# Optimization experiments

Hardware: AMD Instinct MI355X
Metric: run time of the kernel (lower is better)

The kernel has to match this reference:

```python
import jax, jax.numpy as jnp
import numpy as np

N_NODES = 20000
N_EDGES = 320000
INDIM = 64
OUTDIM = 128
EDGE_DIM = 16
HEADS = 4
ED = OUTDIM // 2          # encoded edge dim = 64
C1 = 2 * INDIM // HEADS   # 32 -> concat 128
C2 = OUTDIM // HEADS      # 32 -> concat 128
C3 = 2 * OUTDIM // HEADS  # 64 -> concat 256


def setup_inputs() -> dict:
    key = jax.random.key(0)
    ks = iter(jax.random.split(key, 80))
    def p(*shape):
        return jax.random.normal(next(ks), shape, dtype=jnp.float32) * 0.05
    inp = {}
    inp['x_in'] = jax.random.normal(next(ks), (N_NODES, INDIM), dtype=jnp.float32)
    inp['edge_index'] = jax.random.randint(next(ks), (2, N_EDGES), 0, N_NODES)
    inp['edge_attr'] = jax.random.normal(next(ks), (N_EDGES, EDGE_DIM), dtype=jnp.float32)
    # BatchNorm1d (eval mode: running stats)
    inp['bn0_g'] = jnp.ones(INDIM, jnp.float32) + p(INDIM)
    inp['bn0_b'] = p(INDIM)
    inp['bn0_m'] = p(INDIM)
    inp['bn0_v'] = jnp.ones(INDIM, jnp.float32) + 0.1 * jax.random.uniform(next(ks), (INDIM,))
    # edge encoder: Linear(edge_dim,outdim) -> LeakyReLU -> Linear(outdim,outdim//2) -> LeakyReLU
    inp['ee_W1'] = p(EDGE_DIM, OUTDIM); inp['ee_b1'] = p(OUTDIM)
    inp['ee_W2'] = p(OUTDIM, ED); inp['ee_b2'] = p(ED)
    # GATv2 layers: lin_l, lin_r (bias), lin_edge (no bias), att [H,C], out bias [H*C]
    def gat_params(prefix, din, C):
        inp[prefix + '_Wl'] = p(din, HEADS * C); inp[prefix + '_bl'] = p(HEADS * C)
        inp[prefix + '_Wr'] = p(din, HEADS * C); inp[prefix + '_br'] = p(HEADS * C)
        inp[prefix + '_We'] = p(ED, HEADS * C)
        inp[prefix + '_att'] = p(HEADS, C)
        inp[prefix + '_bias'] = p(HEADS * C)
    gat_params('g1', INDIM, C1)
    gat_params('g2', HEADS * C1, C2)
    gat_params('g3', HEADS * C2, C3)
    # LayerNorms
    inp['ln1_g'] = jnp.ones(HEADS * C1, jnp.float32); inp['ln1_b'] = p(HEADS * C1)
    inp['ln2_g'] = jnp.ones(HEADS * C2, jnp.float32); inp['ln2_b'] = p(HEADS * C2)
    inp['ln3_g'] = jnp.ones(HEADS * C3, jnp.float32); inp['ln3_b'] = p(HEADS * C3)
    # skip / mixing / heads
    inp['skip_W'] = p(INDIM, HEADS * C1); inp['skip_b'] = p(HEADS * C1)
    inp['alpha_p'] = jnp.float32(0.3)
    inp['fp_W'] = p(HEADS * C1, HEADS * C3); inp['fp_b'] = p(HEADS * C3)
    catout = HEADS * C3
    inp['np_W1'] = p(catout, catout // 2); inp['np_b1'] = p(catout // 2)
    inp['np_W2'] = p(catout // 2, catout // 4); inp['np_b2'] = p(catout // 4)
    inp['np_W3'] = p(catout // 4, 1); inp['np_b3'] = p(1)
    return inp


def _ln(x, g, b):
    m = jnp.mean(x, axis=-1, keepdims=True)
    v = jnp.var(x, axis=-1, keepdims=True)
    return (x - m) / jnp.sqrt(v + 1e-5) * g + b


def _gatv2(x, src, dst, ea, Wl, bl, Wr, br, We, att, bias, N):
    # GATv2Conv (eval): e = att . leaky_relu(x_j + x_i + e_ij, 0.2); segment softmax over dst
    H, C = att.shape
    xl = (x @ Wl + bl).reshape(N, H, C)   # source transform
    xr = (x @ Wr + br).reshape(N, H, C)   # target transform
    ee = (ea @ We).reshape(-1, H, C)      # edge transform (no bias)
    m = jax.nn.leaky_relu(xl[src] + xr[dst] + ee, 0.2)  # [E,H,C]
    e = jnp.einsum('ehc,hc->eh', m, att)
    emax = jax.ops.segment_max(e, dst, num_segments=N)
    ex = jnp.exp(e - emax[dst])
    den = jax.ops.segment_sum(ex, dst, num_segments=N)
    alpha = ex / (den[dst] + 1e-16)       # [E,H]
    out = jax.ops.segment_sum(xl[src] * alpha[:, :, None], dst, num_segments=N)
    return out.reshape(N, H * C) + bias, alpha


def reference(x_in, edge_index, edge_attr, bn0_g, bn0_b, bn0_m, bn0_v,
              ee_W1, ee_b1, ee_W2, ee_b2,
              g1_Wl, g1_bl, g1_Wr, g1_br, g1_We, g1_att, g1_bias,
              g2_Wl, g2_bl, g2_Wr, g2_br, g2_We, g2_att, g2_bias,
              g3_Wl, g3_bl, g3_Wr, g3_br, g3_We, g3_att, g3_bias,
              ln1_g, ln1_b, ln2_g, ln2_b, ln3_g, ln3_b,
              skip_W, skip_b, alpha_p, fp_W, fp_b,
              np_W1, np_b1, np_W2, np_b2, np_W3, np_b3):
    N = x_in.shape[0]
    # BatchNorm1d eval
    x = (x_in - bn0_m) / jnp.sqrt(bn0_v + 1e-5) * bn0_g + bn0_b
    # edge encoder + L2 normalize
    ea = jax.nn.leaky_relu(edge_attr @ ee_W1 + ee_b1, 0.01)
    ea = jax.nn.leaky_relu(ea @ ee_W2 + ee_b2, 0.01)
    ea = ea / jnp.maximum(jnp.linalg.norm(ea, axis=-1, keepdims=True), 1e-12)
    # add self loops (fill_value='mean' of incoming encoded edge_attr)
    src0, dst0 = edge_index[0], edge_index[1]
    deg = jax.ops.segment_sum(jnp.ones_like(ea[:, 0]), dst0, num_segments=N)
    loop_attr = jax.ops.segment_sum(ea, dst0, num_segments=N) / jnp.maximum(deg, 1.0)[:, None]
    ar = jnp.arange(N, dtype=src0.dtype)
    src = jnp.concatenate([src0, ar]); dst = jnp.concatenate([dst0, ar])
    ea2 = jnp.concatenate([ea, loop_attr], axis=0)
    x1, a1 = _gatv2(x, src, dst, ea2, g1_Wl, g1_bl, g1_Wr, g1_br, g1_We, g1_att, g1_bias, N)
    x1 = jax.nn.leaky_relu(_ln(x1, ln1_g, ln1_b), 0.01)
    skip1 = 0.01 * (x @ skip_W + skip_b) + x1  # skip_weight = 0.01 (frozen)
    x2, a2 = _gatv2(skip1, src, dst, ea2, g2_Wl, g2_bl, g2_Wr, g2_br, g2_We, g2_att, g2_bias, N)
    x2 = jax.nn.leaky_relu(_ln(x2, ln2_g, ln2_b), 0.01)
    x3, a3 = _gatv2(x2, src, dst, ea2, g3_Wl, g3_bl, g3_Wr, g3_br, g3_We, g3_att, g3_bias, N)
    x3 = jax.nn.leaky_relu(_ln(x3, ln3_g, ln3_b), 0.01)
    s = jax.nn.sigmoid(alpha_p)
    xf = s * (x1 @ fp_W + fp_b) + (1.0 - s) * x3
    h = jax.nn.elu(xf @ np_W1 + np_b1)
    h = jax.nn.elu(h @ np_W2 + np_b2)
    node_probs = h @ np_W3 + np_b3
    return (xf, node_probs, a1, a2, a3)
```

## Files before the change

kernel.cpp:

```cpp
#include <hip/hip_runtime.h>
#include <math.h>

#define DEV __device__ __forceinline__

typedef __attribute__((ext_vector_type(8))) short bf16x8;
typedef __attribute__((ext_vector_type(4))) float f32x4;

DEV float leakyf(float x, float s) { return x > 0.f ? x : s * x; }

DEV unsigned short f2bf(float f) {
  unsigned u = __float_as_uint(f);
  unsigned r = (u + 0x7fff + ((u >> 16) & 1)) >> 16;
  return (unsigned short)r;
}
DEV float bf2f(unsigned short h) { return __uint_as_float((unsigned)h << 16); }

DEV float sel4(float4 v, int h) {
  float a = (h & 1) ? v.y : v.x;
  float b = (h & 1) ? v.w : v.z;
  return (h & 2) ? b : a;
}

DEV float wave_sum(float v) {
#pragma unroll
  for (int o = 1; o < 64; o <<= 1) v += __shfl_xor(v, o);
  return v;
}
DEV float wave_max(float v) {
#pragma unroll
  for (int o = 1; o < 64; o <<= 1) v = fmaxf(v, __shfl_xor(v, o));
  return v;
}

struct WJob { const float* in; unsigned short* out; int K; int Nc; };
struct WJobs { WJob j[13]; };

__global__ __launch_bounds__(256) void wt_kernel(WJobs jobs) {
  WJob jb = jobs.j[blockIdx.y];
  int total = jb.K * jb.Nc;
  for (int i = blockIdx.x * 256 + threadIdx.x; i < total; i += gridDim.x * 256) {
    int c = i / jb.K, k = i - c * jb.K;
    jb.out[i] = f2bf(jb.in[(size_t)k * jb.Nc + c]);
  }
}

__global__ __launch_bounds__(256) void bn_kernel(
    const float* __restrict__ xin, const float* __restrict__ g,
    const float* __restrict__ b, const float* __restrict__ m,
    const float* __restrict__ v, float* __restrict__ xout, int total) {
  int i = blockIdx.x * 256 + threadIdx.x;
  if (i < total) {
    int c = i & 63;
    xout[i] = (xin[i] - m[c]) * rsqrtf(v[c] + 1e-5f) * g[c] + b[c];
  }
}

__global__ __launch_bounds__(256) void edge_enc_kernel(
    const float* __restrict__ edge_attr, const unsigned short* __restrict__ WT1,
    const float* __restrict__ b1, const unsigned short* __restrict__ WT2,
    const float* __restrict__ b2, unsigned short* __restrict__ ea_bf, int E) {
  __shared__ __align__(16) unsigned short sEa1[64][136];
  int tid = threadIdx.x, lane = tid & 63, w = tid >> 6;
  int g = lane >> 4, q = lane & 15;
  bf16x8 w1f[8];
#pragma unroll
  for (int t = 0; t < 8; t++) {
    bf16x8 v = {};
    if (g < 2) v = *(const bf16x8*)(WT1 + (size_t)(16 * t + q) * 16 + 8 * g);
    w1f[t] = v;
  }
  float b1v[8];
#pragma unroll
  for (int t = 0; t < 8; t++) b1v[t] = b1[16 * t + q];
  bf16x8 w2f[4][4];
#pragma unroll
  for (int t = 0; t < 4; t++)
#pragma unroll
    for (int kc = 0; kc < 4; kc++)
      w2f[t][kc] = *(const bf16x8*)(WT2 + (size_t)(16 * t + q) * 128 + 32 * kc + 8 * g);
  float b2v[4];
#pragma unroll
  for (int t = 0; t < 4; t++) b2v[t] = b2[16 * t + q];

  int gstride = gridDim.x * 64;

  auto load_attr = [&](int base) -> bf16x8 {
    bf16x8 af = {};
    if (g < 2) {
      int e = base + w * 16 + q;
      if (e >= E) e = E - 1;
      const float* ap = edge_attr + (size_t)e * 16 + 8 * g;
      float4 x0 = *(const float4*)ap;
      float4 x1 = *(const float4*)(ap + 4);
      af[0] = (short)f2bf(x0.x); af[1] = (short)f2bf(x0.y);
      af[2] = (short)f2bf(x0.z); af[3] = (short)f2bf(x0.w);
      af[4] = (short)f2bf(x1.x); af[5] = (short)f2bf(x1.y);
      af[6] = (short)f2bf(x1.z); af[7] = (short)f2bf(x1.w);
    }
    return af;
  };

  int base = blockIdx.x * 64;
  if (base >= E) return;
  bf16x8 af = load_attr(base);
  for (; base < E; ) {
    int next = base + gstride;
    bf16x8 af_next = {};
    if (next < E) af_next = load_attr(next);
    f32x4 acc1[8];
#pragma unroll
    for (int t = 0; t < 8; t++) acc1[t] = (f32x4){0.f, 0.f, 0.f, 0.f};
#pragma unroll
    for (int t = 0; t < 8; t++)
      acc1[t] = __builtin_amdgcn_mfma_f32_16x16x32_bf16(af, w1f[t], acc1[t], 0, 0, 0);
#pragma unroll
    for (int t = 0; t < 8; t++)
#pragma unroll
      for (int r = 0; r < 4; r++) {
        float v = leakyf(acc1[t][r] + b1v[t], 0.01f);
        sEa1[w * 16 + g * 4 + r][16 * t + q] = f2bf(v);
      }
    f32x4 acc2[4];
#pragma unroll
    for (int t = 0; t < 4; t++) acc2[t] = (f32x4){0.f, 0.f, 0.f, 0.f};
#pragma unroll
    for (int kc = 0; kc < 4; kc++) {
      bf16x8 a2 = *(const bf16x8*)&sEa1[w * 16 + q][32 * kc + 8 * g];
#pragma unroll
      for (int t = 0; t < 4; t++)
        acc2[t] = __builtin_amdgcn_mfma_f32_16x16x32_bf16(a2, w2f[t][kc], acc2[t], 0, 0, 0);
    }
#pragma unroll
    for (int r = 0; r < 4; r++) {
      float vv[4];
      float p = 0.f;
#pragma unroll
      for (int t = 0; t < 4; t++) {
        float v = leakyf(acc2[t][r] + b2v[t], 0.01f);
        vv[t] = v;
        p += v * v;
      }
#pragma unroll
      for (int o = 1; o < 16; o <<= 1) p += __shfl_xor(p, o);
      float sc = 1.f / fmaxf(sqrtf(p), 1e-12f);
#pragma unroll
      for (int t = 0; t < 4; t++)
        sEa1[w * 16 + g * 4 + r][16 * t + q] = f2bf(vv[t] * sc);
    }
#pragma unroll
    for (int p = 0; p < 2; p++) {
      int rl = p * 8 + (lane >> 3);
      int e = base + w * 16 + rl;
      if (e < E) {
        bf16x8 v = *(const bf16x8*)&sEa1[w * 16 + rl][(lane & 7) * 8];
        *(bf16x8*)(ea_bf + (size_t)e * 64 + (lane & 7) * 8) = v;
      }
    }
    af = af_next;
    base = next;
  }
}

__global__ __launch_bounds__(256) void count_kernel(const int* __restrict__ dst0,
                                                    int* __restrict__ counts, int E, int E2) {
  int i = blockIdx.x * 256 + threadIdx.x;
  if (i < E2) {
    int d = (i < E) ? dst0[i] : (i - E);
    atomicAdd(&counts[d], 1);
  }
}

__global__ __launch_bounds__(1024) void scan_kernel(const int* __restrict__ counts,
                                                    int* __restrict__ rowptr,
                                                    int* __restrict__ fill, int N) {
  __shared__ int part[1024];
  int tid = threadIdx.x;
  int chunk = (N + 1023) / 1024;
  int lo = tid * chunk, hi = lo + chunk;
  if (hi > N) hi = N;
  if (lo > N) lo = N;
  int s = 0;
  for (int i = lo; i < hi; i++) s += counts[i];
  part[tid] = s;
  __syncthreads();
#pragma unroll
  for (int o = 1; o < 1024; o <<= 1) {
    int v = (tid >= o) ? part[tid - o] : 0;
    __syncthreads();
    part[tid] += v;
    __syncthreads();
  }
  if (tid == 1023) rowptr[N] = part[1023];
  int off = part[tid] - s;
  for (int i = lo; i < hi; i++) {
    rowptr[i] = off;
    fill[i] = off;
    off += counts[i];
  }
}

__global__ __launch_bounds__(256) void fill_kernel(const int* __restrict__ src0,
                                                   const int* __restrict__ dst0,
                                                   int* __restrict__ fill,
                                                   int* __restrict__ csr,
                                                   int* __restrict__ srcpos,
                                                   int* __restrict__ dstpos, int E, int E2) {
  int i = blockIdx.x * 256 + threadIdx.x;
  if (i < E2) {
    int d, s;
    if (i < E) {
      d = dst0[i];
      s = src0[i];
    } else {
      d = s = i - E;
    }
    int pos = atomicAdd(&fill[d], 1);
    csr[pos] = i;
    srcpos[pos] = s;
    dstpos[pos] = d;
  }
}

__global__ __launch_bounds__(256) void loopattr_kernel(unsigned short* __restrict__ ea_bf,
                                                       const int* __restrict__ rowptr,
                                                       const int* __restrict__ csr, int N, int E) {
  int lane = threadIdx.x & 63, wv = threadIdx.x >> 6;
  int stride = gridDim.x * 4;
  for (int n = blockIdx.x * 4 + wv; n < N; n += stride) {
    int r0 = rowptr[n], r1 = rowptr[n + 1];
    float acc = 0.f;
    int cnt = 0;
    for (int i = r0; i < r1; i++) {
      int e = csr[i];
      if (e < E) {
        acc += bf2f(ea_bf[(size_t)e * 64 + lane]);
        cnt++;
      }
    }
    ea_bf[((size_t)E + n) * 64 + lane] = f2bf(acc / fmaxf((float)cnt, 1.f));
  }
}

template <int MODE>
__global__ __launch_bounds__(256) void gemm_mfma_kernel(
    const float* __restrict__ A, const unsigned short* __restrict__ BT,
    const float* __restrict__ bias, void* __restrict__ Cout, int M, int K, int Nc,
    const float* __restrict__ aux, const float* __restrict__ alpha_p) {
  __shared__ unsigned short sA[64][40];
  __shared__ unsigned short sB[64][40];
  int tid = threadIdx.x, lane = tid & 63, w = tid >> 6;
  int g = lane >> 4, q = lane & 15;
  int bm = blockIdx.y * 64, bn = blockIdx.x * 64;
  f32x4 acc[4];
#pragma unroll
  for (int t = 0; t < 4; t++) acc[t] = (f32x4){0.f, 0.f, 0.f, 0.f};
  int r = tid >> 2, ko = (tid & 3) * 8;
  for (int k0 = 0; k0 < K; k0 += 32) {
    {
      int gm = bm + r;
      bf16x8 v = {};
      if (gm < M) {
        const float* ap = A + (size_t)gm * K + k0 + ko;
        float4 x0 = *(const float4*)ap;
        float4 x1 = *(const float4*)(ap + 4);
        v[0] = (short)f2bf(x0.x); v[1] = (short)f2bf(x0.y);
        v[2] = (short)f2bf(x0.z); v[3] = (short)f2bf(x0.w);
        v[4] = (short)f2bf(x1.x); v[5] = (short)f2bf(x1.y);
        v[6] = (short)f2bf(x1.z); v[7] = (short)f2bf(x1.w);
      }
      *(bf16x8*)&sA[r][ko] = v;
      int gc = bn + r;
      bf16x8 bv = {};
      if (gc < Nc) bv = *(const bf16x8*)(BT + (size_t)gc * K + k0 + ko);
      *(bf16x8*)&sB[r][ko] = bv;
    }
    __syncthreads();
    bf16x8 a = *(const bf16x8*)&sA[w * 16 + q][8 * g];
#pragma unroll
    for (int t = 0; t < 4; t++) {
      bf16x8 b = *(const bf16x8*)&sB[16 * t + q][8 * g];
      acc[t] = __builtin_amdgcn_mfma_f32_16x16x32_bf16(a, b, acc[t], 0, 0, 0);
    }
    __syncthreads();
  }
  float s = 0.f;
  if (MODE == 3) s = 1.f / (1.f + __expf(-alpha_p[0]));
#pragma unroll
  for (int t = 0; t < 4; t++) {
    int col = bn + 16 * t + q;
#pragma unroll
    for (int rr = 0; rr < 4; rr++) {
      int row = bm + w * 16 + g * 4 + rr;
      if (row < M && col < Nc) {
        float v = acc[t][rr] + bias[col];
        if (MODE == 2) v = v > 0.f ? v : (__expf(v) - 1.f);
        if (MODE == 3) v = s * v + (1.f - s) * aux[(size_t)row * Nc + col];
        if (MODE == 1)
          ((unsigned short*)Cout)[(size_t)row * Nc + col] = f2bf(v);
        else
          ((float*)Cout)[(size_t)row * Nc + col] = v;
      }
    }
  }
}

struct GJob { const unsigned short* BT; const float* bias; void* out; int mode; };
struct GJobs { GJob j[3]; };

__global__ __launch_bounds__(256) void gemm_mfma_batched(
    const float* __restrict__ A, GJobs jobs, int M, int K, int Nc) {
  __shared__ unsigned short sA[64][40];
  __shared__ unsigned short sB[64][40];
  GJob jb = jobs.j[blockIdx.z];
  const unsigned short* BT = jb.BT;
  int tid = threadIdx.x, lane = tid & 63, w = tid >> 6;
  int g = lane >> 4, q = lane & 15;
  int bm = blockIdx.y * 64, bn = blockIdx.x * 64;
  f32x4 acc[4];
#pragma unroll
  for (int t = 0; t < 4; t++) acc[t] = (f32x4){0.f, 0.f, 0.f, 0.f};
  int r = tid >> 2, ko = (tid & 3) * 8;
  for (int k0 = 0; k0 < K; k0 += 32) {
    {
      int gm = bm + r;
      bf16x8 v = {};
      if (gm < M) {
        const float* ap = A + (size_t)gm * K + k0 + ko;
        float4 x0 = *(const float4*)ap;
        float4 x1 = *(const float4*)(ap + 4);
        v[0] = (short)f2bf(x0.x); v[1] = (short)f2bf(x0.y);
        v[2] = (short)f2bf(x0.z); v[3] = (short)f2bf(x0.w);
        v[4] = (short)f2bf(x1.x); v[5] = (short)f2bf(x1.y);
        v[6] = (short)f2bf(x1.z); v[7] = (short)f2bf(x1.w);
      }
      *(bf16x8*)&sA[r][ko] = v;
      int gc = bn + r;
      bf16x8 bv = {};
      if (gc < Nc) bv = *(const bf16x8*)(BT + (size_t)gc * K + k0 + ko);
      *(bf16x8*)&sB[r][ko] = bv;
    }
    __syncthreads();
    bf16x8 a = *(const bf16x8*)&sA[w * 16 + q][8 * g];
#pragma unroll
    for (int t = 0; t < 4; t++) {
      bf16x8 b = *(const bf16x8*)&sB[16 * t + q][8 * g];
      acc[t] = __builtin_amdgcn_mfma_f32_16x16x32_bf16(a, b, acc[t], 0, 0, 0);
    }
    __syncthreads();
  }
#pragma unroll
  for (int t = 0; t < 4; t++) {
    int col = bn + 16 * t + q;
#pragma unroll
    for (int rr = 0; rr < 4; rr++) {
      int row = bm + w * 16 + g * 4 + rr;
      if (row < M && col < Nc) {
        float v = acc[t][rr] + jb.bias[col];
        if (jb.mode == 1)
          ((unsigned short*)jb.out)[(size_t)row * Nc + col] = f2bf(v);
        else
          ((float*)jb.out)[(size_t)row * Nc + col] = v;
      }
    }
  }
}

template <int C>
__global__ __launch_bounds__(256) void score_mfma_kernel(
    const unsigned short* __restrict__ ea_bf, const unsigned short* __restrict__ xl,
    const unsigned short* __restrict__ xr, const float* __restrict__ We,
    const float* __restrict__ att, const int* __restrict__ csr,
    const int* __restrict__ srcpos, const int* __restrict__ dstpos,
    float* __restrict__ e_s, int E2, int HCfull, int col_off) {
  int lane = threadIdx.x & 63;
  int wv = threadIdx.x >> 6;
  int g = lane >> 4, q = lane & 15;
  bf16x8 bfrag[8][2];
#pragma unroll
  for (int t = 0; t < 8; t++)
#pragma unroll
    for (int kc = 0; kc < 2; kc++) {
      bf16x8 bv;
#pragma unroll
      for (int j = 0; j < 8; j++) {
        int k = kc * 32 + g * 8 + j;
        bv[j] = (short)f2bf(We[(size_t)k * HCfull + col_off + 16 * t + q]);
      }
      bfrag[t][kc] = bv;
    }
  float attv[8];
#pragma unroll
  for (int t = 0; t < 8; t++) attv[t] = att[col_off + 16 * t + q];

  constexpr int TPH = C / 16;
  constexpr int NH = 8 / TPH;
  const int headbase = col_off / C;

  int tiles = (E2 + 15) / 16;
  int nw = gridDim.x * 4;
  for (int tile = blockIdx.x * 4 + wv; tile < tiles; tile += nw) {
    int i0 = tile * 16;
    int ia = i0 + q;
    if (ia >= E2) ia = E2 - 1;
    int erow = csr[ia];
    const unsigned short* ap = ea_bf + (size_t)erow * 64 + g * 8;
    bf16x8 a0 = *(const bf16x8*)(ap);
    bf16x8 a1 = *(const bf16x8*)(ap + 32);
    f32x4 acc[8];
#pragma unroll
    for (int t = 0; t < 8; t++) acc[t] = (f32x4){0.f, 0.f, 0.f, 0.f};
#pragma unroll
    for (int t = 0; t < 8; t++) {
      acc[t] = __builtin_amdgcn_mfma_f32_16x16x32_bf16(a0, bfrag[t][0], acc[t], 0, 0, 0);
      acc[t] = __builtin_amdgcn_mfma_f32_16x16x32_bf16(a1, bfrag[t][1], acc[t], 0, 0, 0);
    }
    int sn[4], dn[4];
#pragma unroll
    for (int r = 0; r < 4; r++) {
      int i = i0 + g * 4 + r;
      if (i >= E2) i = E2 - 1;
      sn[r] = srcpos[i];
      dn[r] = dstpos[i];
    }
    float p[NH][4];
#pragma unroll
    for (int hh = 0; hh < NH; hh++)
#pragma unroll
      for (int r = 0; r < 4; r++) p[hh][r] = 0.f;
#pragma unroll
    for (int t = 0; t < 8; t++) {
      int col = col_off + 16 * t + q;
#pragma unroll
      for (int r = 0; r < 4; r++) {
        float xv = bf2f(xl[(size_t)sn[r] * HCfull + col]) +
                   bf2f(xr[(size_t)dn[r] * HCfull + col]) + acc[t][r];
        xv = xv > 0.f ? xv : 0.2f * xv;
        p[t / TPH][r] += xv * attv[t];
      }
    }
#pragma unroll
    for (int hh = 0; hh < NH; hh++)
#pragma unroll
      for (int r = 0; r < 4; r++) {
#pragma unroll
        for (int o = 1; o < 16; o <<= 1) p[hh][r] += __shfl_xor(p[hh][r], o);
      }
    if (q == 0) {
#pragma unroll
      for (int r = 0; r < 4; r++) {
        int i = i0 + g * 4 + r;
        if (i < E2) {
#pragma unroll
          for (int hh = 0; hh < NH; hh++)
            e_s[(size_t)i * 4 + headbase + hh] = p[hh][r];
        }
      }
    }
  }
}

template <int HC, bool L1MODE>
__global__ __launch_bounds__(256) void aggr_kernel(
    const float* __restrict__ e_s, const unsigned short* __restrict__ xl,
    const int* __restrict__ rowptr, const int* __restrict__ srcpos,
    const float* __restrict__ bias,
    const float* __restrict__ lng, const float* __restrict__ lnb,
    float* __restrict__ xout,
    float* __restrict__ x1out, const float* __restrict__ skipproj,
    float* __restrict__ md, int N) {
  constexpr int CPL = HC / 64;
  int lane = threadIdx.x & 63, wv = threadIdx.x >> 6;
  int stride = gridDim.x * 4;
  const float4* e_s4 = (const float4*)e_s;
  for (int n = blockIdx.x * 4 + wv; n < N; n += stride) {
    int r0 = rowptr[n], r1 = rowptr[n + 1];
    float m0 = -1e30f, m1 = -1e30f, m2 = -1e30f, m3 = -1e30f;
    for (int i = r0 + lane; i < r1; i += 64) {
      float4 v = e_s4[i];
      m0 = fmaxf(m0, v.x);
      m1 = fmaxf(m1, v.y);
      m2 = fmaxf(m2, v.z);
      m3 = fmaxf(m3, v.w);
    }
    m0 = wave_max(m0);
    m1 = wave_max(m1);
    m2 = wave_max(m2);
    m3 = wave_max(m3);
    float d0 = 0.f, d1 = 0.f, d2 = 0.f, d3 = 0.f;
    for (int i = r0 + lane; i < r1; i += 64) {
      float4 v = e_s4[i];
      d0 += __expf(v.x - m0);
      d1 += __expf(v.y - m1);
      d2 += __expf(v.z - m2);
      d3 += __expf(v.w - m3);
    }
    d0 = wave_sum(d0);
    d1 = wave_sum(d1);
    d2 = wave_sum(d2);
    d3 = wave_sum(d3);
    float i0 = 1.f / (d0 + 1e-16f), i1 = 1.f / (d1 + 1e-16f);
    float i2 = 1.f / (d2 + 1e-16f), i3 = 1.f / (d3 + 1e-16f);
    if (lane == 0) {
      float* mp = md + (size_t)n * 8;
      mp[0] = m0; mp[1] = m1; mp[2] = m2; mp[3] = m3;
      mp[4] = i0; mp[5] = i1; mp[6] = i2; mp[7] = i3;
    }
    int h = lane >> 4;
    float mh = (h & 2) ? ((h & 1) ? m3 : m2) : ((h & 1) ? m1 : m0);
    float ih = (h & 2) ? ((h & 1) ? i3 : i2) : ((h & 1) ? i1 : i0);
    float acc[CPL];
#pragma unroll
    for (int j = 0; j < CPL; j++) acc[j] = 0.f;
    int c0 = lane * CPL;
    int i = r0;
    for (; i + 4 <= r1; i += 4) {
      float sh0, sh1, sh2, sh3;
      int sn0, sn1, sn2, sn3;
      {
        float4 a = e_s4[i], b = e_s4[i + 1], c = e_s4[i + 2], d = e_s4[i + 3];
        sh0 = sel4(a, h); sh1 = sel4(b, h); sh2 = sel4(c, h); sh3 = sel4(d, h);
      }
      sn0 = srcpos[i]; sn1 = srcpos[i + 1]; sn2 = srcpos[i + 2]; sn3 = srcpos[i + 3];
      if constexpr (CPL == 2) {
        ushort2 t0 = *(const ushort2*)(xl + (size_t)sn0 * HC + c0);
        ushort2 t1 = *(const ushort2*)(xl + (size_t)sn1 * HC + c0);
        ushort2 t2 = *(const ushort2*)(xl + (size_t)sn2 * HC + c0);
        ushort2 t3 = *(const ushort2*)(xl + (size_t)sn3 * HC + c0);
        float a0 = __expf(sh0 - mh) * ih;
        float a1 = __expf(sh1 - mh) * ih;
        float a2 = __expf(sh2 - mh) * ih;
        float a3 = __expf(sh3 - mh) * ih;
        acc[0] += a0 * bf2f(t0.x) + a1 * bf2f(t1.x) + a2 * bf2f(t2.x) + a3 * bf2f(t3.x);
        acc[1] += a0 * bf2f(t0.y) + a1 * bf2f(t1.y) + a2 * bf2f(t2.y) + a3 * bf2f(t3.y);
      } else {
        ushort4 t0 = *(const ushort4*)(xl + (size_t)sn0 * HC + c0);
        ushort4 t1 = *(const ushort4*)(xl + (size_t)sn1 * HC + c0);
        ushort4 t2 = *(const ushort4*)(xl + (size_t)sn2 * HC + c0);
        ushort4 t3 = *(const ushort4*)(xl + (size_t)sn3 * HC + c0);
        float a0 = __expf(sh0 - mh) * ih;
        float a1 = __expf(sh1 - mh) * ih;
        float a2 = __expf(sh2 - mh) * ih;
        float a3 = __expf(sh3 - mh) * ih;
        acc[0] += a0 * bf2f(t0.x) + a1 * bf2f(t1.x) + a2 * bf2f(t2.x) + a3 * bf2f(t3.x);
        acc[1] += a0 * bf2f(t0.y) + a1 * bf2f(t1.y) + a2 * bf2f(t2.y) + a3 * bf2f(t3.y);
        acc[2] += a0 * bf2f(t0.z) + a1 * bf2f(t1.z) + a2 * bf2f(t2.z) + a3 * bf2f(t3.z);
        acc[3] += a0 * bf2f(t0.w) + a1 * bf2f(t1.w) + a2 * bf2f(t2.w) + a3 * bf2f(t3.w);
      }
    }
    for (; i < r1; i++) {
      float sh = sel4(e_s4[i], h);
      float a = __expf(sh - mh) * ih;
      int sn = srcpos[i];
      const unsigned short* xp = xl + (size_t)sn * HC + c0;
      if constexpr (CPL == 2) {
        ushort2 t = *(const ushort2*)xp;
        acc[0] += a * bf2f(t.x);
        acc[1] += a * bf2f(t.y);
      } else {
        ushort4 t = *(const ushort4*)xp;
        acc[0] += a * bf2f(t.x);
        acc[1] += a * bf2f(t.y);
        acc[2] += a * bf2f(t.z);
        acc[3] += a * bf2f(t.w);
      }
    }
    float vals[CPL];
    float vs = 0.f, vq = 0.f;
#pragma unroll
    for (int j = 0; j < CPL; j++) {
      float t = acc[j] + bias[c0 + j];
      vals[j] = t;
      vs += t;
      vq += t * t;
    }
    vs = wave_sum(vs);
    vq = wave_sum(vq);
    float mean = vs * (1.f / HC);
    float var = vq * (1.f / HC) - mean * mean;
    float rstd = rsqrtf(fmaxf(var, 0.f) + 1e-5f);
#pragma unroll
    for (int j = 0; j < CPL; j++) {
      int c = c0 + j;
      float y = (vals[j] - mean) * rstd * lng[c] + lnb[c];
      y = leakyf(y, 0.01f);
      if constexpr (L1MODE) {
        x1out[(size_t)n * HC + c] = y;
        xout[(size_t)n * HC + c] = 0.01f * skipproj[(size_t)n * HC + c] + y;
      } else {
        xout[(size_t)n * HC + c] = y;
      }
    }
  }
}

__global__ __launch_bounds__(256) void alpha_kernel(
    const float* __restrict__ e_s, const int* __restrict__ csr,
    const int* __restrict__ dstpos, const float* __restrict__ md,
    float* __restrict__ alpha_out, int E2) {
  int i = blockIdx.x * 256 + threadIdx.x;
  if (i < E2) {
    float4 sv = ((const float4*)e_s)[i];
    int d = dstpos[i];
    const float* mp = md + (size_t)d * 8;
    float4 a;
    a.x = __expf(sv.x - mp[0]) * mp[4];
    a.y = __expf(sv.y - mp[1]) * mp[5];
    a.z = __expf(sv.z - mp[2]) * mp[6];
    a.w = __expf(sv.w - mp[3]) * mp[7];
    ((float4*)alpha_out)[csr[i]] = a;
  }
}

extern "C" void kernel_launch(void* const* d_in, const int* in_sizes, int n_in,
                              void* d_out, int out_size, void* d_ws, size_t ws_size,
                              hipStream_t stream) {
  (void)n_in;
  (void)out_size;
  (void)ws_size;
  const float* x_in = (const float*)d_in[0];
  const int* edge_index = (const int*)d_in[1];
  const float* edge_attr = (const float*)d_in[2];
  const float* bn0_g = (const float*)d_in[3];
  const float* bn0_b = (const float*)d_in[4];
  const float* bn0_m = (const float*)d_in[5];
  const float* bn0_v = (const float*)d_in[6];
  const float* eeW1 = (const float*)d_in[7];
  const float* eeb1 = (const float*)d_in[8];
  const float* eeW2 = (const float*)d_in[9];
  const float* eeb2 = (const float*)d_in[10];
  const float* g1_Wl = (const float*)d_in[11];
  const float* g1_bl = (const float*)d_in[12];
  const float* g1_Wr = (const float*)d_in[13];
  const float* g1_br = (const float*)d_in[14];
  const float* g1_We = (const float*)d_in[15];
  const float* g1_att = (const float*)d_in[16];
  const float* g1_bias = (const float*)d_in[17];
  const float* g2_Wl = (const float*)d_in[18];
  const float* g2_bl = (const float*)d_in[19];
  const float* g2_Wr = (const float*)d_in[20];
  const float* g2_br = (const float*)d_in[21];
  const float* g2_We = (const float*)d_in[22];
  const float* g2_att = (const float*)d_in[23];
  const float* g2_bias = (const float*)d_in[24];
  const float* g3_Wl = (const float*)d_in[25];
  const float* g3_bl = (const float*)d_in[26];
  const float* g3_Wr = (const float*)d_in[27];
  const float* g3_br = (const float*)d_in[28];
  const float* g3_We = (const float*)d_in[29];
  const float* g3_att = (const float*)d_in[30];
  const float* g3_bias = (const float*)d_in[31];
  const float* ln1_g = (const float*)d_in[32];
  const float* ln1_b = (const float*)d_in[33];
  const float* ln2_g = (const float*)d_in[34];
  const float* ln2_b = (const float*)d_in[35];
  const float* ln3_g = (const float*)d_in[36];
  const float* ln3_b = (const float*)d_in[37];
  const float* skip_W = (const float*)d_in[38];
  const float* skip_b = (const float*)d_in[39];
  const float* alpha_p = (const float*)d_in[40];
  const float* fp_W = (const float*)d_in[41];
  const float* fp_b = (const float*)d_in[42];
  const float* np_W1 = (const float*)d_in[43];
  const float* np_b1 = (const float*)d_in[44];
  const float* np_W2 = (const float*)d_in[45];
  const float* np_b2 = (const float*)d_in[46];
  const float* np_W3 = (const float*)d_in[47];
  const float* np_b3 = (const float*)d_in[48];

  const int N = in_sizes[0] / 64;
  const int E = in_sizes[2] / 16;
  const int E2 = E + N;
  const int* src0 = edge_index;
  const int* dst0 = edge_index + E;

  float* ws = (float*)d_ws;
  size_t off = 0;
  float* x = ws + off;         off += (size_t)N * 64;
  unsigned short* ea_bf = (unsigned short*)(ws + off); off += (size_t)E2 * 32;
  unsigned short* xl = (unsigned short*)(ws + off);    off += (size_t)N * 128;
  unsigned short* xr = (unsigned short*)(ws + off);    off += (size_t)N * 128;
  float* skipproj = ws + off;  off += (size_t)N * 128;
  float* x1 = ws + off;        off += (size_t)N * 128;
  float* skip1 = ws + off;     off += (size_t)N * 128;
  float* x2 = ws + off;        off += (size_t)N * 128;
  float* x3 = ws + off;        off += (size_t)N * 256;
  float* e_s = ws + off;       off += (size_t)E2 * 4;
  float* h2 = ws + off;        off += (size_t)N * 64;
  float* md = ws + off;        off += (size_t)N * 8;
  int* counts = (int*)(ws + off);
  int* rowptr = counts + N;
  int* fill = rowptr + N + 1;
  int* csr = fill + N;
  int* srcpos = csr + E2;
  int* dstpos = srcpos + E2;
  off += (size_t)(3 * N + 1 + 3 * E2);
  off = (off + 3) & ~(size_t)3;
  unsigned short* wtp = (unsigned short*)(ws + off);
  auto alloc_wt = [&](int elems) {
    unsigned short* p = wtp;
    wtp += (elems + 7) & ~7;
    return p;
  };
  unsigned short* wt_g1l = alloc_wt(64 * 128);
  unsigned short* wt_g1r = alloc_wt(64 * 128);
  unsigned short* wt_skip = alloc_wt(64 * 128);
  unsigned short* wt_g2l = alloc_wt(128 * 128);
  unsigned short* wt_g2r = alloc_wt(128 * 128);
  unsigned short* wt_g3l = alloc_wt(128 * 256);
  unsigned short* wt_g3r = alloc_wt(128 * 256);
  unsigned short* wt_fp = alloc_wt(128 * 256);
  unsigned short* wt_np1 = alloc_wt(256 * 128);
  unsigned short* wt_np2 = alloc_wt(128 * 64);
  unsigned short* wt_np3 = alloc_wt(64 * 1);
  unsigned short* wt_ee1 = alloc_wt(16 * 128);
  unsigned short* wt_ee2 = alloc_wt(128 * 64);

  float* out = (float*)d_out;
  float* xf = out;
  float* npout = out + (size_t)N * 256;
  float* a1 = npout + N;
  float* a2 = a1 + (size_t)E2 * 4;
  float* a3 = a2 + (size_t)E2 * 4;

  WJobs jobs;
  jobs.j[0] = {g1_Wl, wt_g1l, 64, 128};
  jobs.j[1] = {g1_Wr, wt_g1r, 64, 128};
  jobs.j[2] = {skip_W, wt_skip, 64, 128};
  jobs.j[3] = {g2_Wl, wt_g2l, 128, 128};
  jobs.j[4] = {g2_Wr, wt_g2r, 128, 128};
  jobs.j[5] = {g3_Wl, wt_g3l, 128, 256};
  jobs.j[6] = {g3_Wr, wt_g3r, 128, 256};
  jobs.j[7] = {fp_W, wt_fp, 128, 256};
  jobs.j[8] = {np_W1, wt_np1, 256, 128};
  jobs.j[9] = {np_W2, wt_np2, 128, 64};
  jobs.j[10] = {np_W3, wt_np3, 64, 1};
  jobs.j[11] = {eeW1, wt_ee1, 16, 128};
  jobs.j[12] = {eeW2, wt_ee2, 128, 64};

  hipMemsetAsync(counts, 0, (size_t)N * sizeof(int), stream);
  wt_kernel<<<dim3(64, 13), 256, 0, stream>>>(jobs);
  bn_kernel<<<(N * 64 + 255) / 256, 256, 0, stream>>>(x_in, bn0_g, bn0_b, bn0_m, bn0_v, x, N * 64);
  edge_enc_kernel<<<2560, 256, 0, stream>>>(edge_attr, wt_ee1, eeb1, wt_ee2, eeb2, ea_bf, E);
  count_kernel<<<(E2 + 255) / 256, 256, 0, stream>>>(dst0, counts, E, E2);
  scan_kernel<<<1, 1024, 0, stream>>>(counts, rowptr, fill, N);
  fill_kernel<<<(E2 + 255) / 256, 256, 0, stream>>>(src0, dst0, fill, csr, srcpos, dstpos, E, E2);
  loopattr_kernel<<<(N + 3) / 4, 256, 0, stream>>>(ea_bf, rowptr, csr, N, E);

  auto gemm = [&](int mode, const float* A, const unsigned short* BT, const float* bias,
                  void* Cp, int M, int K, int Nc, const float* aux) {
    dim3 gdim((Nc + 63) / 64, (M + 63) / 64);
    switch (mode) {
      case 0: gemm_mfma_kernel<0><<<gdim, 256, 0, stream>>>(A, BT, bias, Cp, M, K, Nc, nullptr, nullptr); break;
      case 2: gemm_mfma_kernel<2><<<gdim, 256, 0, stream>>>(A, BT, bias, Cp, M, K, Nc, nullptr, nullptr); break;
      case 3: gemm_mfma_kernel<3><<<gdim, 256, 0, stream>>>(A, BT, bias, Cp, M, K, Nc, aux, alpha_p); break;
    }
  };
  auto gemm_batch = [&](const float* A, int M, int K, int Nc, GJobs gj, int nz) {
    dim3 gdim((Nc + 63) / 64, (M + 63) / 64, nz);
    gemm_mfma_batched<<<gdim, 256, 0, stream>>>(A, gj, M, K, Nc);
  };

  const int nblk_node = (N + 3) / 4;
  const int score_blocks = 1024;
  const int nblk_edge = (E2 + 255) / 256;

  {
    GJobs gj;
    gj.j[0] = {wt_g1l, g1_bl, xl, 1};
    gj.j[1] = {wt_g1r, g1_br, xr, 1};
    gj.j[2] = {wt_skip, skip_b, skipproj, 0};
    gemm_batch(x, N, 64, 128, gj, 3);
  }
  score_mfma_kernel<32><<<score_blocks, 256, 0, stream>>>(ea_bf, xl, xr, g1_We, g1_att, csr, srcpos, dstpos, e_s, E2, 128, 0);
  aggr_kernel<128, true><<<nblk_node, 256, 0, stream>>>(e_s, xl, rowptr, srcpos, g1_bias, ln1_g, ln1_b,
                                                        skip1, x1, skipproj, md, N);
  alpha_kernel<<<nblk_edge, 256, 0, stream>>>(e_s, csr, dstpos, md, a1, E2);
  {
    GJobs gj;
    gj.j[0] = {wt_g2l, g2_bl, xl, 1};
    gj.j[1] = {wt_g2r, g2_br, xr, 1};
    gj.j[2] = {nullptr, nullptr, nullptr, 0};
    gemm_batch(skip1, N, 128, 128, gj, 2);
  }
  score_mfma_kernel<32><<<score_blocks, 256, 0, stream>>>(ea_bf, xl, xr, g2_We, g2_att, csr, srcpos, dstpos, e_s, E2, 128, 0);
  aggr_kernel<128, false><<<nblk_node, 256, 0, stream>>>(e_s, xl, rowptr, srcpos, g2_bias, ln2_g, ln2_b,
                                                         x2, nullptr, nullptr, md, N);
  alpha_kernel<<<nblk_edge, 256, 0, stream>>>(e_s, csr, dstpos, md, a2, E2);
  {
    GJobs gj;
    gj.j[0] = {wt_g3l, g3_bl, xl, 1};
    gj.j[1] = {wt_g3r, g3_br, xr, 1};
    gj.j[2] = {nullptr, nullptr, nullptr, 0};
    gemm_batch(x2, N, 128, 256, gj, 2);
  }
  score_mfma_kernel<64><<<score_blocks, 256, 0, stream>>>(ea_bf, xl, xr, g3_We, g3_att, csr, srcpos, dstpos, e_s, E2, 256, 0);
  score_mfma_kernel<64><<<score_blocks, 256, 0, stream>>>(ea_bf, xl, xr, g3_We, g3_att, csr, srcpos, dstpos, e_s, E2, 256, 128);
  aggr_kernel<256, false><<<nblk_node, 256, 0, stream>>>(e_s, xl, rowptr, srcpos, g3_bias, ln3_g, ln3_b,
                                                         x3, nullptr, nullptr, md, N);
  alpha_kernel<<<nblk_edge, 256, 0, stream>>>(e_s, csr, dstpos, md, a3, E2);
  gemm(3, x1, wt_fp, fp_b, xf, N, 128, 256, x3);
  gemm(2, xf, wt_np1, np_b1, skipproj, N, 256, 128, nullptr);
  gemm(2, skipproj, wt_np2, np_b2, h2, N, 128, 64, nullptr);
  gemm(0, h2, wt_np3, np_b3, npout, N, 64, 1, nullptr);
}
```

Baseline: 530.5 us.

## Merge layer-3 score kernels into one split launch and simplify edge encoder output

Layer 3's two score launches, one per 128-column half, become a single launch. In it, wave pairs cover the two column halves of the same edge tile, so both halves share the gathered edge attributes and node features in cache. The edge encoder now writes normalized outputs straight to global memory with scalar bf16 stores instead of staging them through shared memory for vectorized stores. It also gets a launch-bounds occupancy hint and half the grid size. The direct stores are narrow and less coalesced, which could cost more than the dropped shared-memory round trip saves.

```diff
diff --git a/kernel.cpp b/kernel.cpp
--- a/kernel.cpp
+++ b/kernel.cpp
@@ -55,11 +55,11 @@
   }
 }
 
-__global__ __launch_bounds__(256) void edge_enc_kernel(
+__global__ __launch_bounds__(256, 2) void edge_enc_kernel(
     const float* __restrict__ edge_attr, const unsigned short* __restrict__ WT1,
     const float* __restrict__ b1, const unsigned short* __restrict__ WT2,
     const float* __restrict__ b2, unsigned short* __restrict__ ea_bf, int E) {
-  __shared__ __align__(16) unsigned short sEa1[64][136];
+  __shared__ unsigned short sEa1[64][136];
   int tid = threadIdx.x, lane = tid & 63, w = tid >> 6;
   int g = lane >> 4, q = lane & 15;
   bf16x8 w1f[8];
@@ -107,6 +107,7 @@
     int next = base + gstride;
     bf16x8 af_next = {};
     if (next < E) af_next = load_attr(next);
+    int e0 = base + w * 16;
     f32x4 acc1[8];
 #pragma unroll
     for (int t = 0; t < 8; t++) acc1[t] = (f32x4){0.f, 0.f, 0.f, 0.f};
@@ -143,17 +144,11 @@
 #pragma unroll
       for (int o = 1; o < 16; o <<= 1) p += __shfl_xor(p, o);
       float sc = 1.f / fmaxf(sqrtf(p), 1e-12f);
-#pragma unroll
-      for (int t = 0; t < 4; t++)
-        sEa1[w * 16 + g * 4 + r][16 * t + q] = f2bf(vv[t] * sc);
-    }
-#pragma unroll
-    for (int p = 0; p < 2; p++) {
-      int rl = p * 8 + (lane >> 3);
-      int e = base + w * 16 + rl;
+      int e = e0 + g * 4 + r;
       if (e < E) {
-        bf16x8 v = *(const bf16x8*)&sEa1[w * 16 + rl][(lane & 7) * 8];
-        *(bf16x8*)(ea_bf + (size_t)e * 64 + (lane & 7) * 8) = v;
+#pragma unroll
+        for (int t = 0; t < 4; t++)
+          ea_bf[(size_t)e * 64 + 16 * t + q] = f2bf(vv[t] * sc);
       }
     }
     af = af_next;
@@ -365,16 +360,17 @@
   }
 }
 
-template <int C>
+template <int C, bool SPLIT>
 __global__ __launch_bounds__(256) void score_mfma_kernel(
     const unsigned short* __restrict__ ea_bf, const unsigned short* __restrict__ xl,
     const unsigned short* __restrict__ xr, const float* __restrict__ We,
     const float* __restrict__ att, const int* __restrict__ csr,
     const int* __restrict__ srcpos, const int* __restrict__ dstpos,
-    float* __restrict__ e_s, int E2, int HCfull, int col_off) {
+    float* __restrict__ e_s, int E2, int HCfull, int col_off_in) {
   int lane = threadIdx.x & 63;
   int wv = threadIdx.x >> 6;
   int g = lane >> 4, q = lane & 15;
+  int col_off = SPLIT ? (wv & 1) * 128 : col_off_in;
   bf16x8 bfrag[8][2];
 #pragma unroll
   for (int t = 0; t < 8; t++)
@@ -397,8 +393,9 @@
   const int headbase = col_off / C;
 
   int tiles = (E2 + 15) / 16;
-  int nw = gridDim.x * 4;
-  for (int tile = blockIdx.x * 4 + wv; tile < tiles; tile += nw) {
+  int tstart = SPLIT ? (blockIdx.x * 2 + (wv >> 1)) : (blockIdx.x * 4 + wv);
+  int nw = SPLIT ? (gridDim.x * 2) : (gridDim.x * 4);
+  for (int tile = tstart; tile < tiles; tile += nw) {
     int i0 = tile * 16;
     int ia = i0 + q;
     if (ia >= E2) ia = E2 - 1;
@@ -740,7 +737,7 @@
   hipMemsetAsync(counts, 0, (size_t)N * sizeof(int), stream);
   wt_kernel<<<dim3(64, 13), 256, 0, stream>>>(jobs);
   bn_kernel<<<(N * 64 + 255) / 256, 256, 0, stream>>>(x_in, bn0_g, bn0_b, bn0_m, bn0_v, x, N * 64);
-  edge_enc_kernel<<<2560, 256, 0, stream>>>(edge_attr, wt_ee1, eeb1, wt_ee2, eeb2, ea_bf, E);
+  edge_enc_kernel<<<1280, 256, 0, stream>>>(edge_attr, wt_ee1, eeb1, wt_ee2, eeb2, ea_bf, E);
   count_kernel<<<(E2 + 255) / 256, 256, 0, stream>>>(dst0, counts, E, E2);
   scan_kernel<<<1, 1024, 0, stream>>>(counts, rowptr, fill, N);
   fill_kernel<<<(E2 + 255) / 256, 256, 0, stream>>>(src0, dst0, fill, csr, srcpos, dstpos, E, E2);
@@ -771,7 +768,7 @@
     gj.j[2] = {wt_skip, skip_b, skipproj, 0};
     gemm_batch(x, N, 64, 128, gj, 3);
   }
-  score_mfma_kernel<32><<<score_blocks, 256, 0, stream>>>(ea_bf, xl, xr, g1_We, g1_att, csr, srcpos, dstpos, e_s, E2, 128, 0);
+  score_mfma_kernel<32, false><<<score_blocks, 256, 0, stream>>>(ea_bf, xl, xr, g1_We, g1_att, csr, srcpos, dstpos, e_s, E2, 128, 0);
   aggr_kernel<128, true><<<nblk_node, 256, 0, stream>>>(e_s, xl, rowptr, srcpos, g1_bias, ln1_g, ln1_b,
                                                         skip1, x1, skipproj, md, N);
   alpha_kernel<<<nblk_edge, 256, 0, stream>>>(e_s, csr, dstpos, md, a1, E2);
@@ -782,7 +779,7 @@
     gj.j[2] = {nullptr, nullptr, nullptr, 0};
     gemm_batch(skip1, N, 128, 128, gj, 2);
   }
-  score_mfma_kernel<32><<<score_blocks, 256, 0, stream>>>(ea_bf, xl, xr, g2_We, g2_att, csr, srcpos, dstpos, e_s, E2, 128, 0);
+  score_mfma_kernel<32, false><<<score_blocks, 256, 0, stream>>>(ea_bf, xl, xr, g2_We, g2_att, csr, srcpos, dstpos, e_s, E2, 128, 0);
   aggr_kernel<128, false><<<nblk_node, 256, 0, stream>>>(e_s, xl, rowptr, srcpos, g2_bias, ln2_g, ln2_b,
                                                          x2, nullptr, nullptr, md, N);
   alpha_kernel<<<nblk_edge, 256, 0, stream>>>(e_s, csr, dstpos, md, a2, E2);
@@ -793,8 +790,7 @@
     gj.j[2] = {nullptr, nullptr, nullptr, 0};
     gemm_batch(x2, N, 128, 256, gj, 2);
   }
-  score_mfma_kernel<64><<<score_blocks, 256, 0, stream>>>(ea_bf, xl, xr, g3_We, g3_att, csr, srcpos, dstpos, e_s, E2, 256, 0);
-  score_mfma_kernel<64><<<score_blocks, 256, 0, stream>>>(ea_bf, xl, xr, g3_We, g3_att, csr, srcpos, dstpos, e_s, E2, 256, 128);
+  score_mfma_kernel<64, true><<<score_blocks, 256, 0, stream>>>(ea_bf, xl, xr, g3_We, g3_att, csr, srcpos, dstpos, e_s, E2, 256, 0);
   aggr_kernel<256, false><<<nblk_node, 256, 0, stream>>>(e_s, xl, rowptr, srcpos, g3_bias, ln3_g, ln3_b,
                                                          x3, nullptr, nullptr, md, N);
   alpha_kernel<<<nblk_edge, 256, 0, stream>>>(e_s, csr, dstpos, md, a3, E2);
```

New measurement: 505.7 us. 1.05x faster.
